# Performance work log

Measured on AMD Instinct MI355X. Metric: run time of the kernel, lower is better.

## Reference

```python
import jax, jax.numpy as jnp
import numpy as np

N = 100000      # nodes
E = 1600000     # edges
D_IN = 256
D_HID = 256
D_OUT = 256
DROP_P = 0.5


def setup_inputs() -> dict:
    key = jax.random.key(0)
    ks = jax.random.split(key, 10)
    s = 1.0 / np.sqrt(D_HID)
    return {
        "z": jax.random.normal(ks[0], (N, D_OUT), jnp.float32),
        "omega": jax.random.normal(ks[1], (N, D_IN), jnp.float32),
        "edge_index": jax.random.randint(ks[2], (2, E), 0, N, jnp.int32),
        "W_lin": jax.random.normal(ks[3], (D_IN, D_HID), jnp.float32) * s,
        "b_lin": jnp.zeros((D_HID,), jnp.float32),
        "W_g1": jax.random.normal(ks[4], (D_HID, D_HID), jnp.float32) * s,
        "b_g1": jnp.zeros((D_HID,), jnp.float32),
        "W_g2": jax.random.normal(ks[5], (D_HID, D_OUT), jnp.float32) * s,
        "b_g2": jnp.zeros((D_OUT,), jnp.float32),
        "mask1": jax.random.bernoulli(ks[6], 1.0 - DROP_P, (N, D_HID)),
        "mask2": jax.random.bernoulli(ks[7], 1.0 - DROP_P, (N, D_HID)),
    }


def _gcn_norm(edge_index):
    # add self-loops, symmetric normalization deg^-1/2 * deg^-1/2
    loop = jnp.arange(N, dtype=edge_index.dtype)
    src = jnp.concatenate([edge_index[0], loop])
    dst = jnp.concatenate([edge_index[1], loop])
    deg = jax.ops.segment_sum(jnp.ones_like(dst, jnp.float32), dst, num_segments=N)
    dinv = jax.lax.rsqrt(deg)  # deg >= 1 because of self-loops
    norm = dinv[src] * dinv[dst]  # [E+N]
    return src, dst, norm


def _gcn_conv(x, W, b, src, dst, norm):
    h = x @ W                                  # [N, d_out]
    msg = h[src] * norm[:, None]               # gather over edges
    out = jax.ops.segment_sum(msg, dst, num_segments=N)  # scatter-add
    return out + b


def _dropout(x, mask):
    return jnp.where(mask, x * (1.0 / (1.0 - DROP_P)), 0.0)


def reference(z, omega, edge_index, W_lin, b_lin, W_g1, b_g1, W_g2, b_g2, mask1, mask2):
    src, dst, norm = _gcn_norm(edge_index)
    # layer 0: Linear + relu + dropout
    h = _dropout(jax.nn.relu(omega @ W_lin + b_lin), mask1)
    # layer 1: GCNConv + relu + dropout
    h = _dropout(jax.nn.relu(_gcn_conv(h, W_g1, b_g1, src, dst, norm)), mask2)
    # layer 2: GCNConv
    h = _gcn_conv(h, W_g2, b_g2, src, dst, norm)
    return z * h
```

## Files before the change

kernel.cpp:

```cpp
#include <hip/hip_runtime.h>
#include <stdint.h>

#define NN 100000
#define EE 1600000
#define DD 256

typedef __bf16 bf16;
typedef __attribute__((ext_vector_type(8))) __bf16 bf16x8;
typedef __attribute__((ext_vector_type(4))) float f32x4;
typedef __attribute__((ext_vector_type(4))) unsigned int u32x4;
typedef __attribute__((ext_vector_type(8))) unsigned short u16x8;

typedef __attribute__((address_space(1))) const unsigned int g_u32c;
typedef __attribute__((address_space(3))) unsigned int lds_u32;

__device__ __forceinline__ float bflo(unsigned int u) {
    union { unsigned int u; float f; } x; x.u = u << 16; return x.f;
}
__device__ __forceinline__ float bfhi(unsigned int u) {
    union { unsigned int u; float f; } x; x.u = u & 0xFFFF0000u; return x.f;
}
__device__ __forceinline__ unsigned short f2bf(float f) {
    return __builtin_bit_cast(unsigned short, (__bf16)f);
}

__global__ void count_deg_k(const int* __restrict__ dst, int* __restrict__ cnt) {
    int e = blockIdx.x * 256 + threadIdx.x;
    if (e < EE) atomicAdd(&cnt[dst[e]], 1);
}
__global__ __launch_bounds__(256) void scan_blk_k(const int* __restrict__ cnt,
                                                  int* __restrict__ part,
                                                  int* __restrict__ bsum,
                                                  float* __restrict__ dinv) {
    __shared__ int buf[256];
    int i = blockIdx.x * 256 + threadIdx.x;
    int v = 0;
    if (i < NN) { v = cnt[i] + 1; dinv[i] = rsqrtf((float)v); }
    buf[threadIdx.x] = v;
    __syncthreads();
    for (int off = 1; off < 256; off <<= 1) {
        int t = (threadIdx.x >= off) ? buf[threadIdx.x - off] : 0;
        __syncthreads();
        buf[threadIdx.x] += t;
        __syncthreads();
    }
    if (i < NN) part[i] = buf[threadIdx.x];
    if (threadIdx.x == 255) bsum[blockIdx.x] = buf[255];
}
__global__ __launch_bounds__(512) void scan_top_k(const int* __restrict__ bsum,
                                                  int* __restrict__ bpre, int nb) {
    __shared__ int buf[512];
    int v = (threadIdx.x < (unsigned)nb) ? bsum[threadIdx.x] : 0;
    buf[threadIdx.x] = v;
    __syncthreads();
    for (int off = 1; off < 512; off <<= 1) {
        int t = (threadIdx.x >= off) ? buf[threadIdx.x - off] : 0;
        __syncthreads();
        buf[threadIdx.x] += t;
        __syncthreads();
    }
    if (threadIdx.x < (unsigned)nb) bpre[threadIdx.x] = buf[threadIdx.x] - v;
}
__global__ void scan_fin_k(const int* __restrict__ part, const int* __restrict__ bpre,
                           const int* __restrict__ cnt,
                           int* __restrict__ offs, int* __restrict__ cur,
                           int* __restrict__ cs) {
    int i = blockIdx.x * 256 + threadIdx.x;
    if (i >= NN) return;
    int o1 = part[i] + bpre[blockIdx.x];
    offs[i + 1] = o1;
    if (i == 0) offs[0] = 0;
    int o = o1 - (cnt[i] + 1);
    cs[o] = i;
    cur[i] = o + 1;
}
#define NSUB 128
__global__ __launch_bounds__(256) void fill_csr_k(
    const int* __restrict__ src, const int* __restrict__ dst,
    int* __restrict__ cur, int* __restrict__ cs) {
    int bid = blockIdx.x;
    int prt = bid & 7;
    int sub = bid >> 3;
    int lo = prt * (NN >> 3);
    int hi = (prt == 7) ? NN : lo + (NN >> 3);
    const int per = EE / NSUB;
    int e0 = sub * per;
    int e1 = (sub == NSUB - 1) ? EE : e0 + per;
    for (int e = e0 + threadIdx.x; e < e1; e += 256) {
        int d = dst[e];
        if (d >= lo && d < hi) {
            int s = src[e];
            int pos = atomicAdd(&cur[d], 1);
            cs[pos] = s;
        }
    }
}

__global__ __launch_bounds__(256) void prep_k(
    const float* __restrict__ W0, const float* __restrict__ W1, const float* __restrict__ W2,
    bf16* __restrict__ T0, bf16* __restrict__ T1, bf16* __restrict__ T2,
    const unsigned int* __restrict__ m, int* __restrict__ flag) {
    int b = blockIdx.x;
    if (b == 192) {
        if (threadIdx.x < 64) {
            unsigned int v = m[threadIdx.x];
            int bad = (v > 1u && v != 0x3F800000u) ? 1 : 0;
            unsigned long long bl = __ballot(bad);
            if (threadIdx.x == 0) *flag = (bl != 0ull) ? 1 : 0;
        }
        return;
    }
    const float* W = b < 64 ? W0 : (b < 128 ? W1 : W2);
    bf16*       T  = b < 64 ? T0 : (b < 128 ? T1 : T2);
    int bb = b & 63;
    __shared__ float tile[32][33];
    int bx = bb & 7, by = bb >> 3;
    int tx = threadIdx.x & 31, ty = threadIdx.x >> 5;
    #pragma unroll
    for (int r = 0; r < 32; r += 8)
        tile[ty + r][tx] = W[(size_t)(by * 32 + ty + r) * DD + bx * 32 + tx];
    __syncthreads();
    #pragma unroll
    for (int r = 0; r < 32; r += 8)
        T[(size_t)(bx * 32 + ty + r) * DD + by * 32 + tx] = (bf16)tile[tx][ty + r];
}

__global__ void cvt_rows_k(const float* __restrict__ in, unsigned short* __restrict__ out) {
    int i = blockIdx.x * 256 + threadIdx.x;
    float4 v = ((const float4*)in)[i];
    ushort4 o = { f2bf(v.x), f2bf(v.y), f2bf(v.z), f2bf(v.w) };
    ((ushort4*)out)[i] = o;
}

template <int ID, int EPI>
__global__ __launch_bounds__(256) void gemm_k(
    const bf16* __restrict__ A, const bf16* __restrict__ Wt,
    const float* __restrict__ bias, const void* __restrict__ mask,
    const int* __restrict__ flagp, const float* __restrict__ z,
    const float* __restrict__ dinv, void* __restrict__ outp) {
    __shared__ __align__(16) bf16 As[128 * 64];
    __shared__ __align__(16) bf16 Bs[128 * 64];

    int bid = blockIdx.x;
    int m   = ((bid >> 4) << 3) | (bid & 7);
    int h   = (bid >> 3) & 1;
    int m0  = m * 128, n0 = h * 128;
    if (m0 >= NN) return;
    int tid = threadIdx.x;
    int wid = tid >> 6, lane = tid & 63;
    int wm = wid >> 1, wn = wid & 1;
    int lr = lane & 15, lk = lane >> 4;

    f32x4 acc[4][4] = {};

    for (int k0 = 0; k0 < DD; k0 += 64) {
        #pragma unroll
        for (int i = 0; i < 4; i++) {
            int f = i * 256 + tid;
            int row = f >> 3;
            int c   = (f & 7) * 8;
            int gr = m0 + row; if (gr > NN - 1) gr = NN - 1;
            __builtin_amdgcn_global_load_lds(
                (g_u32c*)(A + (size_t)gr * DD + k0 + c),
                (lds_u32*)(As + (size_t)f * 8), 16, 0, 0);
            __builtin_amdgcn_global_load_lds(
                (g_u32c*)(Wt + (size_t)(n0 + row) * DD + k0 + c),
                (lds_u32*)(Bs + (size_t)f * 8), 16, 0, 0);
        }
        __syncthreads();
        #pragma unroll
        for (int kk = 0; kk < 2; kk++) {
            bf16x8 af[4], bfr[4];
            #pragma unroll
            for (int mi = 0; mi < 4; mi++)
                af[mi] = *(const bf16x8*)(As + (wm * 64 + mi * 16 + lr) * 64 + kk * 32 + lk * 8);
            #pragma unroll
            for (int ni = 0; ni < 4; ni++)
                bfr[ni] = *(const bf16x8*)(Bs + (wn * 64 + ni * 16 + lr) * 64 + kk * 32 + lk * 8);
            #pragma unroll
            for (int mi = 0; mi < 4; mi++)
                #pragma unroll
                for (int ni = 0; ni < 4; ni++)
                    acc[mi][ni] = __builtin_amdgcn_mfma_f32_16x16x32_bf16(
                        bfr[ni], af[mi], acc[mi][ni], 0, 0, 0);
        }
        __syncthreads();
    }

    int bm = (EPI == 1) ? *flagp : 0;
    #pragma unroll
    for (int mi = 0; mi < 4; mi++) {
        int gr = m0 + wm * 64 + mi * 16 + lr;
        if (gr >= NN) continue;
        float ds = (EPI == 1) ? dinv[gr] : 0.f;
        #pragma unroll
        for (int ni = 0; ni < 4; ni++) {
            int gc = n0 + wn * 64 + ni * 16 + lk * 4;
            size_t idx = (size_t)gr * DD + gc;
            float4 b4 = *(const float4*)(bias + gc);
            float v0 = acc[mi][ni][0] + b4.x;
            float v1 = acc[mi][ni][1] + b4.y;
            float v2 = acc[mi][ni][2] + b4.z;
            float v3 = acc[mi][ni][3] + b4.w;
            if (EPI == 1) {
                v0 = fmaxf(v0, 0.f); v1 = fmaxf(v1, 0.f);
                v2 = fmaxf(v2, 0.f); v3 = fmaxf(v3, 0.f);
                if (bm) {
                    uchar4 u = *(const uchar4*)((const unsigned char*)mask + idx);
                    v0 *= u.x ? 2.f : 0.f; v1 *= u.y ? 2.f : 0.f;
                    v2 *= u.z ? 2.f : 0.f; v3 *= u.w ? 2.f : 0.f;
                } else {
                    uint4 u = *(const uint4*)((const unsigned int*)mask + idx);
                    v0 *= u.x ? 2.f : 0.f; v1 *= u.y ? 2.f : 0.f;
                    v2 *= u.z ? 2.f : 0.f; v3 *= u.w ? 2.f : 0.f;
                }
                v0 *= ds; v1 *= ds; v2 *= ds; v3 *= ds;
                ushort4 o = { f2bf(v0), f2bf(v1), f2bf(v2), f2bf(v3) };
                *(ushort4*)((unsigned short*)outp + idx) = o;
            } else {
                f32x4 zz = __builtin_nontemporal_load((const f32x4*)(z + idx));
                f32x4 o = { v0 * zz.x, v1 * zz.y, v2 * zz.z, v3 * zz.w };
                __builtin_nontemporal_store(o, (f32x4*)((float*)outp + idx));
            }
        }
    }
}

#define AGG_GET(J, UVAR, MVAR)                                                   \
    {                                                                            \
        int _i = 2 * (J) + half;                                                 \
        int _s = __shfl(sl, _i & 63);                                            \
        MVAR = (_i < nume) ? 1.f : 0.f;                                          \
        UVAR = *(const u32x4*)(tb + (((size_t)(unsigned)_s) << 9) + lcoff);      \
    }
#define AGG_FMA(UVAR, MVAR)                                                      \
    {                                                                            \
        acc[0] = fmaf(MVAR, bflo(UVAR.x), acc[0]);                               \
        acc[1] = fmaf(MVAR, bfhi(UVAR.x), acc[1]);                               \
        acc[2] = fmaf(MVAR, bflo(UVAR.y), acc[2]);                               \
        acc[3] = fmaf(MVAR, bfhi(UVAR.y), acc[3]);                               \
        acc[4] = fmaf(MVAR, bflo(UVAR.z), acc[4]);                               \
        acc[5] = fmaf(MVAR, bfhi(UVAR.z), acc[5]);                               \
        acc[6] = fmaf(MVAR, bflo(UVAR.w), acc[6]);                               \
        acc[7] = fmaf(MVAR, bfhi(UVAR.w), acc[7]);                               \
    }

__global__ __launch_bounds__(256) void agg_k(
    const bf16* __restrict__ t, const int* __restrict__ offs,
    const int* __restrict__ cs, const float* __restrict__ dinv,
    bf16* __restrict__ out) {
    int node = blockIdx.x * 4 + (threadIdx.x >> 6);
    if (node >= NN) return;
    int lane = threadIdx.x & 63;
    int half = lane >> 5;
    int lc = lane & 31;
    int beg = offs[node], end = offs[node + 1];

    float acc[8] = {};
    const char* tb = (const char*)t;
    size_t lcoff = (size_t)(lc << 4);

    for (int base = beg; base < end; base += 64) {
        int nume = min(64, end - base);
        int sl = 0;
        if (lane < nume) sl = __builtin_nontemporal_load(cs + base + lane);
        int nit = (nume + 1) >> 1;

        u32x4 ua, ub, uc, ud;
        float ma, mb, mc, md;
        AGG_GET(0, ua, ma);
        AGG_GET(1, ub, mb);
        AGG_GET(2, uc, mc);
        int j = 0;
        for (; j + 3 < nit; j += 4) {
            AGG_GET(j + 3, ud, md); AGG_FMA(ua, ma);
            AGG_GET(j + 4, ua, ma); AGG_FMA(ub, mb);
            AGG_GET(j + 5, ub, mb); AGG_FMA(uc, mc);
            AGG_GET(j + 6, uc, mc); AGG_FMA(ud, md);
        }
        int rem = nit - j;
        if (rem > 0) AGG_FMA(ua, ma);
        if (rem > 1) AGG_FMA(ub, mb);
        if (rem > 2) AGG_FMA(uc, mc);
    }

    float dn = dinv[node];
    #pragma unroll
    for (int i = 0; i < 8; i++) {
        acc[i] += __shfl_xor(acc[i], 32);
        acc[i] *= dn;
    }
    if (half == 0) {
        u16x8 o = { f2bf(acc[0]), f2bf(acc[1]), f2bf(acc[2]), f2bf(acc[3]),
                    f2bf(acc[4]), f2bf(acc[5]), f2bf(acc[6]), f2bf(acc[7]) };
        __builtin_nontemporal_store(o, (u16x8*)((unsigned short*)out + (size_t)node * DD + lc * 8));
    }
}

extern "C" void kernel_launch(void* const* d_in, const int* in_sizes, int n_in,
                              void* d_out, int out_size, void* d_ws, size_t ws_size,
                              hipStream_t stream) {
    const float* z     = (const float*)d_in[0];
    const float* omega = (const float*)d_in[1];
    const int*   eidx  = (const int*)d_in[2];
    const float* W_lin = (const float*)d_in[3];
    const float* b_lin = (const float*)d_in[4];
    const float* W_g1  = (const float*)d_in[5];
    const float* b_g1  = (const float*)d_in[6];
    const float* W_g2  = (const float*)d_in[7];
    const float* b_g2  = (const float*)d_in[8];
    const void*  mask1 = d_in[9];
    const void*  mask2 = d_in[10];

    const int* e_src = eidx;
    const int* e_dst = eidx + EE;

    char* p = (char*)d_ws;
    size_t off = 0;
    auto alloc = [&](size_t bytes) -> char* {
        char* r = p + off;
        off = (off + bytes + 255) & ~(size_t)255;
        return r;
    };
    const int NB256 = (NN + 255) / 256;
    int*   flag = (int*)  alloc(4);
    int*   cnt  = (int*)  alloc((size_t)NN * 4);
    int*   offs = (int*)  alloc(((size_t)NN + 1) * 4);
    int*   cur  = (int*)  alloc((size_t)NN * 4);
    int*   part = (int*)  alloc((size_t)NN * 4);
    int*   bsum = (int*)  alloc(512 * 4);
    int*   bpre = (int*)  alloc(512 * 4);
    float* dinv = (float*)alloc((size_t)NN * 4);
    int*   cs   = (int*)  alloc((size_t)(EE + NN) * 4);
    bf16*  WtL  = (bf16*) alloc((size_t)DD * DD * 2);
    bf16*  Wt1  = (bf16*) alloc((size_t)DD * DD * 2);
    bf16*  Wt2  = (bf16*) alloc((size_t)DD * DD * 2);
    const size_t NBH = (size_t)NN * DD * 2;
    bf16*  S1   = (bf16*) alloc(NBH);
    bf16*  S2   = (bf16*) alloc(NBH);
    bf16*  S0   = (bf16*)d_out;

    (void)hipMemsetAsync(cnt, 0, (size_t)NN * 4, stream);
    count_deg_k<<<EE / 256, 256, 0, stream>>>(e_dst, cnt);
    scan_blk_k <<<NB256, 256, 0, stream>>>(cnt, part, bsum, dinv);
    scan_top_k <<<1, 512, 0, stream>>>(bsum, bpre, NB256);
    scan_fin_k <<<NB256, 256, 0, stream>>>(part, bpre, cnt, offs, cur, cs);
    fill_csr_k <<<NSUB * 8, 256, 0, stream>>>(e_src, e_dst, cur, cs);

    prep_k<<<193, 256, 0, stream>>>(W_lin, W_g1, W_g2, WtL, Wt1, Wt2,
                                    (const unsigned int*)mask1, flag);
    cvt_rows_k<<<NN * DD / 4 / 256, 256, 0, stream>>>(omega, (unsigned short*)S0);

    const int GG = 1568;
    gemm_k<0, 1><<<GG, 256, 0, stream>>>(S0, WtL, b_lin, mask1, flag, nullptr, dinv, S1);
    agg_k<<<NN / 4, 256, 0, stream>>>(S1, offs, cs, dinv, S2);
    gemm_k<1, 1><<<GG, 256, 0, stream>>>(S2, Wt1, b_g1, mask2, flag, nullptr, dinv, S1);
    agg_k<<<NN / 4, 256, 0, stream>>>(S1, offs, cs, dinv, S2);
    gemm_k<2, 2><<<GG, 256, 0, stream>>>(S2, Wt2, b_g2, nullptr, flag, z, dinv, d_out);
}
```

Baseline: 623.7 us.

## Fuse fp32-to-bf16 input conversion into GEMM and widen blocks to full N

Removes the separate omega conversion kernel by converting fp32 rows to bf16 while staging the A tile in the first GEMM. Each GEMM block now computes all 256 output columns with 512 threads, so A rows are loaded once instead of once per column half. This reduces global memory traffic and one launch. In exchange, the fp32 A load goes through registers instead of async global-to-LDS, and LDS per block grows.

```diff
diff --git a/kernel.cpp b/kernel.cpp
--- a/kernel.cpp
+++ b/kernel.cpp
@@ -125,49 +125,64 @@
         T[(size_t)(bx * 32 + ty + r) * DD + by * 32 + tx] = (bf16)tile[tx][ty + r];
 }
 
-__global__ void cvt_rows_k(const float* __restrict__ in, unsigned short* __restrict__ out) {
-    int i = blockIdx.x * 256 + threadIdx.x;
-    float4 v = ((const float4*)in)[i];
-    ushort4 o = { f2bf(v.x), f2bf(v.y), f2bf(v.z), f2bf(v.w) };
-    ((ushort4*)out)[i] = o;
-}
-
-template <int ID, int EPI>
-__global__ __launch_bounds__(256) void gemm_k(
-    const bf16* __restrict__ A, const bf16* __restrict__ Wt,
+template <int ID, int EPI, int F32A>
+__global__ __launch_bounds__(512, 2) void gemm_k(
+    const void* __restrict__ Ap, const bf16* __restrict__ Wt,
     const float* __restrict__ bias, const void* __restrict__ mask,
     const int* __restrict__ flagp, const float* __restrict__ z,
     const float* __restrict__ dinv, void* __restrict__ outp) {
     __shared__ __align__(16) bf16 As[128 * 64];
-    __shared__ __align__(16) bf16 Bs[128 * 64];
-
-    int bid = blockIdx.x;
-    int m   = ((bid >> 4) << 3) | (bid & 7);
-    int h   = (bid >> 3) & 1;
-    int m0  = m * 128, n0 = h * 128;
+    __shared__ __align__(16) bf16 Bs[256 * 64];
+
+    int m0 = blockIdx.x * 128;
     if (m0 >= NN) return;
     int tid = threadIdx.x;
     int wid = tid >> 6, lane = tid & 63;
-    int wm = wid >> 1, wn = wid & 1;
+    int wm = wid >> 2, wn = wid & 3;
     int lr = lane & 15, lk = lane >> 4;
 
     f32x4 acc[4][4] = {};
 
     for (int k0 = 0; k0 < DD; k0 += 64) {
+        if (F32A) {
+            const float* Af = (const float*)Ap;
+            #pragma unroll
+            for (int i = 0; i < 2; i++) {
+                int f = i * 512 + tid;
+                int row = f >> 3;
+                int c   = (f & 7) * 8;
+                int gr = m0 + row; if (gr > NN - 1) gr = NN - 1;
+                const float* sp = Af + (size_t)gr * DD + k0 + c;
+                float4 v0 = *(const float4*)sp;
+                float4 v1 = *(const float4*)(sp + 4);
+                u16x8 o = { f2bf(v0.x), f2bf(v0.y), f2bf(v0.z), f2bf(v0.w),
+                            f2bf(v1.x), f2bf(v1.y), f2bf(v1.z), f2bf(v1.w) };
+                *(u16x8*)(As + row * 64 + c) = o;
+            }
+        } else {
+            const bf16* Ab = (const bf16*)Ap;
+            #pragma unroll
+            for (int i = 0; i < 2; i++) {
+                int f = i * 512 + tid;
+                int row = f >> 3;
+                int c   = (f & 7) * 8;
+                int gr = m0 + row; if (gr > NN - 1) gr = NN - 1;
+                __builtin_amdgcn_global_load_lds(
+                    (g_u32c*)(Ab + (size_t)gr * DD + k0 + c),
+                    (lds_u32*)(As + (size_t)f * 8), 16, 0, 0);
+            }
+        }
         #pragma unroll
         for (int i = 0; i < 4; i++) {
-            int f = i * 256 + tid;
+            int f = i * 512 + tid;
             int row = f >> 3;
             int c   = (f & 7) * 8;
-            int gr = m0 + row; if (gr > NN - 1) gr = NN - 1;
             __builtin_amdgcn_global_load_lds(
-                (g_u32c*)(A + (size_t)gr * DD + k0 + c),
-                (lds_u32*)(As + (size_t)f * 8), 16, 0, 0);
-            __builtin_amdgcn_global_load_lds(
-                (g_u32c*)(Wt + (size_t)(n0 + row) * DD + k0 + c),
+                (g_u32c*)(Wt + (size_t)row * DD + k0 + c),
                 (lds_u32*)(Bs + (size_t)f * 8), 16, 0, 0);
         }
         __syncthreads();
+
         #pragma unroll
         for (int kk = 0; kk < 2; kk++) {
             bf16x8 af[4], bfr[4];
@@ -195,7 +210,7 @@
         float ds = (EPI == 1) ? dinv[gr] : 0.f;
         #pragma unroll
         for (int ni = 0; ni < 4; ni++) {
-            int gc = n0 + wn * 64 + ni * 16 + lk * 4;
+            int gc = wn * 64 + ni * 16 + lk * 4;
             size_t idx = (size_t)gr * DD + gc;
             float4 b4 = *(const float4*)(bias + gc);
             float v0 = acc[mi][ni][0] + b4.x;
@@ -338,7 +353,6 @@
     const size_t NBH = (size_t)NN * DD * 2;
     bf16*  S1   = (bf16*) alloc(NBH);
     bf16*  S2   = (bf16*) alloc(NBH);
-    bf16*  S0   = (bf16*)d_out;
 
     (void)hipMemsetAsync(cnt, 0, (size_t)NN * 4, stream);
     count_deg_k<<<EE / 256, 256, 0, stream>>>(e_dst, cnt);
@@ -349,12 +363,11 @@
 
     prep_k<<<193, 256, 0, stream>>>(W_lin, W_g1, W_g2, WtL, Wt1, Wt2,
                                     (const unsigned int*)mask1, flag);
-    cvt_rows_k<<<NN * DD / 4 / 256, 256, 0, stream>>>(omega, (unsigned short*)S0);
-
-    const int GG = 1568;
-    gemm_k<0, 1><<<GG, 256, 0, stream>>>(S0, WtL, b_lin, mask1, flag, nullptr, dinv, S1);
+
+    const int GB = (NN + 127) / 128;
+    gemm_k<0, 1, 1><<<GB, 512, 0, stream>>>(omega, WtL, b_lin, mask1, flag, nullptr, dinv, S1);
     agg_k<<<NN / 4, 256, 0, stream>>>(S1, offs, cs, dinv, S2);
-    gemm_k<1, 1><<<GG, 256, 0, stream>>>(S2, Wt1, b_g1, mask2, flag, nullptr, dinv, S1);
+    gemm_k<1, 1, 0><<<GB, 512, 0, stream>>>(S2, Wt1, b_g1, mask2, flag, nullptr, dinv, S1);
     agg_k<<<NN / 4, 256, 0, stream>>>(S1, offs, cs, dinv, S2);
-    gemm_k<2, 2><<<GG, 256, 0, stream>>>(S2, Wt2, b_g2, nullptr, flag, z, dinv, d_out);
-}
+    gemm_k<2, 2, 0><<<GB, 512, 0, stream>>>(S2, Wt2, b_g2, nullptr, flag, z, dinv, d_out);
+}
```

New measurement: 656.4 us. +5.2%, slower.
